# Performance work log

Measured on AMD Instinct MI355X. Metric: run time of the kernel, lower is better.

Reference implementation:

```python
import jax, jax.numpy as jnp
import numpy as np

B, L, T, LM, DFF, D, H = 8, 256, 2048, 4096, 1024, 84, 4
HD = D // H  # 21
NCLS = 265


def _ln(x, s, b):
    m = x.mean(-1, keepdims=True)
    v = ((x - m) ** 2).mean(-1, keepdims=True)
    return (x - m) * jax.lax.rsqrt(v + 1e-5) * s + b


def _fourier(xyz, gB):
    # PositionEmbeddingCoordsSine(d_pos=10, pos_type='fourier'): xyz @ B * 2pi -> [sin, cos]
    proj = (2.0 * jnp.pi) * jnp.einsum('bnc,cd->bnd', xyz, gB)  # [B,N,5]
    return jnp.concatenate([jnp.sin(proj), jnp.cos(proj)], axis=-1)  # [B,N,10]


def setup_inputs() -> dict:
    key = jax.random.key(0)
    ks = jax.random.split(key, 20)
    def nrm(k, shape, scale):
        return jax.random.normal(k, shape, jnp.float32) * scale
    coords = jax.random.uniform(ks[0], (B, L, 6), jnp.float32)
    cls = jax.random.randint(ks[1], (B, L), 0, NCLS).astype(jnp.float32)
    vision_features = jnp.concatenate([coords, cls[..., None]], axis=-1)  # [B,L,7]
    FIN = D * L + LM  # 25600
    inp = {
        'grd_tokens': nrm(ks[2], (T, LM), 1.0),
        'vision_features': vision_features,
        'token_batch_idx': jax.random.randint(ks[3], (T,), 0, B),
        'gauss_B': nrm(ks[4], (3, 5), 1.0),
        'class_emb': nrm(ks[5], (NCLS, 64), 0.02),
        'w_in': nrm(ks[6], (2, D, 3 * D), D ** -0.5),
        'b_in': jnp.zeros((2, 3 * D), jnp.float32),
        'w_out': nrm(ks[7], (2, D, D), D ** -0.5),
        'b_out': jnp.zeros((2, D), jnp.float32),
        'ln1_s': jnp.ones((2, D), jnp.float32), 'ln1_b': jnp.zeros((2, D), jnp.float32),
        'w_ff1': nrm(ks[8], (2, D, DFF), D ** -0.5), 'b_ff1': jnp.zeros((2, DFF), jnp.float32),
        'w_ff2': nrm(ks[9], (2, DFF, D), DFF ** -0.5), 'b_ff2': jnp.zeros((2, D), jnp.float32),
        'ln2_s': jnp.ones((2, D), jnp.float32), 'ln2_b': jnp.zeros((2, D), jnp.float32),
        'w0': nrm(ks[10], (FIN, DFF), FIN ** -0.5), 'b0': jnp.zeros((DFF,), jnp.float32),
        'w1': nrm(ks[11], (DFF, DFF), DFF ** -0.5), 'b1': jnp.zeros((DFF,), jnp.float32),
        'w2': nrm(ks[12], (DFF, DFF), DFF ** -0.5), 'b2': jnp.zeros((DFF,), jnp.float32),
        'w3': nrm(ks[13], (DFF, DFF), DFF ** -0.5), 'b3': jnp.zeros((DFF,), jnp.float32),
        'w4': nrm(ks[14], (DFF, 6), DFF ** -0.5), 'b4': jnp.zeros((6,), jnp.float32),
    }
    return inp


def reference(grd_tokens, vision_features, token_batch_idx, gauss_B, class_emb,
              w_in, b_in, w_out, b_out, ln1_s, ln1_b, w_ff1, b_ff1, w_ff2, b_ff2,
              ln2_s, ln2_b, w0, b0, w1, b1, w2, b2, w3, b3, w4, b4):
    pe_min = _fourier(vision_features[:, :, 0:3], gauss_B)  # [B,L,10]
    pe_max = _fourier(vision_features[:, :, 3:6], gauss_B)  # [B,L,10]
    cls = vision_features[:, :, -1].astype(jnp.int32)
    src = jnp.concatenate([pe_min, pe_max, class_emb[cls]], axis=-1)  # [B,L,84]
    pad = jnp.all(vision_features == 0, axis=-1)  # [B,L]
    neg = jnp.where(pad, -1e9, 0.0)[:, None, None, :]  # [B,1,1,L] key-padding bias
    # 2-layer post-norm transformer encoder (DETR-style, pos=None, dropout=0)
    for l in range(2):
        qkv = src @ w_in[l] + b_in[l]
        q, k, v = jnp.split(qkv, 3, axis=-1)
        q = q.reshape(B, L, H, HD)
        k = k.reshape(B, L, H, HD)
        v = v.reshape(B, L, H, HD)
        scores = jnp.einsum('blhd,bmhd->bhlm', q, k) / jnp.sqrt(jnp.float32(HD)) + neg
        attn = jax.nn.softmax(scores, axis=-1)
        o = jnp.einsum('bhlm,bmhd->blhd', attn, v).reshape(B, L, D)
        src = _ln(src + o @ w_out[l] + b_out[l], ln1_s[l], ln1_b[l])
        ff = jax.nn.relu(src @ w_ff1[l] + b_ff1[l]) @ w_ff2[l] + b_ff2[l]
        src = _ln(src + ff, ln2_s[l], ln2_b[l])
    vision_flat = src.reshape(B, L * D)  # flattened encoder output per sample [B, 21504]
    # batched version of the ragged python loop: gather per-token vision feat + concat lm feat
    feat = jnp.concatenate([vision_flat[token_batch_idx], grd_tokens], axis=-1)  # [T, 25600]
    h = jax.nn.relu(feat @ w0 + b0)
    h = jax.nn.relu(h @ w1 + b1)
    h = jax.nn.relu(h @ w2 + b2)
    h = jax.nn.relu(h @ w3 + b3)
    return h @ w4 + b4  # [T, 6]
```

## Files before the change

### kernel.cpp

```cpp
#include <hip/hip_runtime.h>
#include <hip/hip_bf16.h>

#define B_ 8
#define L_ 256
#define T_ 2048
#define LM_ 4096
#define DFF_ 1024
#define D_ 84
#define H_ 4
#define HD_ 21
#define BL_ (B_*L_)
#define VISF_ (L_*D_)
#define VKS 168
#define VCHUNK (VISF_/VKS)
#define AKS 8
#define AKEYS (L_/AKS)

typedef __attribute__((ext_vector_type(8))) short bf16x8;
typedef __attribute__((ext_vector_type(4))) float f32x4;

struct bh4 { __hip_bfloat16 x, y, z, w; };


__device__ __forceinline__ void dev_wT_pack(const float* __restrict__ W,
        __hip_bfloat16* __restrict__ Wp, int K, int N, int kb, int nb, int tid,
        float (*t)[33])
{
    int tx = tid & 31, ty = tid >> 5;
    #pragma unroll
    for (int i = 0; i < 4; ++i)
        t[ty + i*8][tx] = W[(size_t)(kb + ty + i*8)*N + nb + tx];
    __syncthreads();
    int KG = K >> 3;
    #pragma unroll
    for (int i = 0; i < 4; ++i) {
        int n = nb + ty + i*8, k = kb + tx;
        Wp[((size_t)(n>>4)*KG + (k>>3))*128 + (n&15)*8 + (k&7)] = __float2bfloat16(t[tx][ty + i*8]);
    }
}

__device__ __forceinline__ void dev_wTp_pack(const float* __restrict__ W,
        __hip_bfloat16* __restrict__ Wp, int K, int N, int KP, int kb, int nb, int tid,
        float (*t)[33])
{
    int tx = tid & 31, ty = tid >> 5;
    #pragma unroll
    for (int i = 0; i < 4; ++i) {
        int k = kb + ty + i*8, n = nb + tx;
        t[ty + i*8][tx] = (k < K && n < N) ? W[(size_t)k*N + n] : 0.0f;
    }
    __syncthreads();
    int KG = KP >> 3;
    #pragma unroll
    for (int i = 0; i < 4; ++i) {
        int n = nb + ty + i*8, k = kb + tx;
        Wp[((size_t)(n>>4)*KG + (k>>3))*128 + (n&15)*8 + (k&7)] = __float2bfloat16(t[tx][ty + i*8]);
    }
}

__device__ __forceinline__ void dev_f2b_pack(const float* __restrict__ in,
        __hip_bfloat16* __restrict__ out, int i)
{
    int row = i >> 9, kc = i & 511;
    const float4* p = reinterpret_cast<const float4*>(in + (size_t)row*4096 + kc*8);
    float4 v0 = p[0], v1 = p[1];
    bh4 a = { __float2bfloat16(v0.x), __float2bfloat16(v0.y),
              __float2bfloat16(v0.z), __float2bfloat16(v0.w) };
    bh4 b = { __float2bfloat16(v1.x), __float2bfloat16(v1.y),
              __float2bfloat16(v1.z), __float2bfloat16(v1.w) };
    __hip_bfloat16* o = out + ((size_t)(row>>4)*512 + kc)*128 + (row&15)*8;
    reinterpret_cast<bh4*>(o)[0] = a;
    reinterpret_cast<bh4*>(o)[1] = b;
}

__device__ __forceinline__ void dev_build_src(const float* __restrict__ vf,
        const float* __restrict__ gB, const float* __restrict__ cemb,
        float* __restrict__ src, float* __restrict__ neg, int row)
{
    float v[7];
    bool allz = true;
    #pragma unroll
    for (int c = 0; c < 7; ++c) { v[c] = vf[row*7 + c]; allz = allz && (v[c] == 0.0f); }
    neg[row] = allz ? -1e9f : 0.0f;
    float* s = src + (size_t)row * D_;
    const float TWO_PI = 6.28318530717958647692f;
    #pragma unroll
    for (int d = 0; d < 5; ++d) {
        float pmin = TWO_PI * (v[0]*gB[d] + v[1]*gB[5+d] + v[2]*gB[10+d]);
        float pmax = TWO_PI * (v[3]*gB[d] + v[4]*gB[5+d] + v[5]*gB[10+d]);
        s[d]      = sinf(pmin);  s[5+d]  = cosf(pmin);
        s[10+d]   = sinf(pmax);  s[15+d] = cosf(pmax);
    }
    int cls = (int)v[6];
    const float4* ce = reinterpret_cast<const float4*>(cemb + (size_t)cls*64);
    float4* so = reinterpret_cast<float4*>(s + 20);
    #pragma unroll
    for (int i = 0; i < 16; ++i) so[i] = ce[i];
}

__global__ __launch_bounds__(256) void k_pack_all(
        const float* __restrict__ grd, const float* __restrict__ w0,
        const float* __restrict__ w1, const float* __restrict__ w2,
        const float* __restrict__ w3, const float* __restrict__ w_ff1,
        const float* __restrict__ w_ff2,
        const float* __restrict__ vf, const float* __restrict__ gB,
        const float* __restrict__ cemb,
        __hip_bfloat16* __restrict__ grdb, __hip_bfloat16* __restrict__ w0t,
        __hip_bfloat16* __restrict__ w1t, __hip_bfloat16* __restrict__ w2t,
        __hip_bfloat16* __restrict__ w3t, __hip_bfloat16* __restrict__ wff1t,
        __hip_bfloat16* __restrict__ wff2t,
        float* __restrict__ src, float* __restrict__ neg)
{
    __shared__ float t[32][33];
    int blk = blockIdx.x, tid = threadIdx.x;
    if (blk < 4096) {
        dev_wT_pack(w0 + (size_t)VISF_*DFF_, w0t, LM_, DFF_,
                    (blk & 127)*32, (blk >> 7)*32, tid, t);
    } else if (blk < 5120) {
        int u = blk - 4096;
        dev_wT_pack(w1, w1t, DFF_, DFF_, (u & 31)*32, (u >> 5)*32, tid, t);
    } else if (blk < 6144) {
        int u = blk - 5120;
        dev_wT_pack(w2, w2t, DFF_, DFF_, (u & 31)*32, (u >> 5)*32, tid, t);
    } else if (blk < 7168) {
        int u = blk - 6144;
        dev_wT_pack(w3, w3t, DFF_, DFF_, (u & 31)*32, (u >> 5)*32, tid, t);
    } else if (blk < 7424) {
        int u = blk - 7168;
        int l = u >> 7; u &= 127;
        dev_wTp_pack(w_ff1 + (size_t)l*D_*DFF_, wff1t + (size_t)l*1024*128,
                     D_, DFF_, 128, (u & 3)*32, (u >> 2)*32, tid, t);
    } else if (blk < 7616) {
        int u = blk - 7424;
        int l = u / 96; u -= l*96;
        dev_wTp_pack(w_ff2 + (size_t)l*DFF_*D_, wff2t + (size_t)l*98304,
                     DFF_, D_, DFF_, (u % 32)*32, (u / 32)*32, tid, t);
    } else if (blk < 11712) {
        dev_f2b_pack(grd, grdb, (blk - 7616)*256 + tid);
    } else {
        dev_build_src(vf, gB, cemb, src, neg, (blk - 11712)*256 + tid);
    }
}

__global__ __launch_bounds__(256) void k_qkv8(const float* __restrict__ src,
        const float* __restrict__ w_in, const float* __restrict__ b_in,
        float* __restrict__ qkv, int lay)
{
    __shared__ float s8[8][D_];
    int r0 = blockIdx.x * 8, tid = threadIdx.x;
    for (int idx = tid; idx < 8*D_; idx += 256) {
        int r = idx / D_, d = idx - r*D_;
        s8[r][d] = src[(size_t)(r0+r)*D_ + d];
    }
    __syncthreads();
    if (tid < 3*D_) {
        const float* w = w_in + (size_t)lay*D_*3*D_ + tid;
        float acc[8] = {};
        for (int d = 0; d < D_; ++d) {
            float wv = w[(size_t)d*3*D_];
            #pragma unroll
            for (int r = 0; r < 8; ++r) acc[r] = fmaf(s8[r][d], wv, acc[r]);
        }
        float bv = b_in[lay*3*D_ + tid];
        #pragma unroll
        for (int r = 0; r < 8; ++r) qkv[(size_t)(r0+r)*(3*D_) + tid] = acc[r] + bv;
    }
}

__global__ __launch_bounds__(256) void k_attn_part(const float* __restrict__ qkv,
        const float* __restrict__ neg, float* __restrict__ part)
{
    __shared__ float ks_[AKEYS*HD_], vs_[AKEYS*HD_], ns[AKEYS];
    int bh = blockIdx.x;
    int b = bh >> 2, h = bh & 3;
    int sp = blockIdx.y;
    int tid = threadIdx.x;
    int k0 = sp * AKEYS;
    for (int idx = tid; idx < AKEYS*HD_; idx += 256) {
        int l = idx / HD_, d = idx - l*HD_;
        size_t base = ((size_t)(b*L_ + k0 + l))*(3*D_) + h*HD_ + d;
        ks_[idx] = qkv[base + D_];
        vs_[idx] = qkv[base + 2*D_];
    }
    if (tid < AKEYS) ns[tid] = neg[b*L_ + k0 + tid];
    __syncthreads();
    float q[HD_];
    {
        size_t base = ((size_t)(b*L_ + tid))*(3*D_) + h*HD_;
        #pragma unroll
        for (int d = 0; d < HD_; ++d) q[d] = qkv[base + d];
    }
    const float scale = 0.21821789023599239f;
    float m_run = -INFINITY, l_run = 0.0f;
    float o[HD_];
    #pragma unroll
    for (int d = 0; d < HD_; ++d) o[d] = 0.0f;
    for (int m = 0; m < AKEYS; ++m) {
        const float* krow = &ks_[m*HD_];
        float sdot = 0.0f;
        #pragma unroll
        for (int d = 0; d < HD_; ++d) sdot = fmaf(q[d], krow[d], sdot);
        float sc = sdot * scale + ns[m];
        float nm = fmaxf(m_run, sc);
        float c = __expf(m_run - nm);
        float p = __expf(sc - nm);
        l_run = l_run * c + p;
        const float* vrow = &vs_[m*HD_];
        #pragma unroll
        for (int d = 0; d < HD_; ++d) o[d] = fmaf(p, vrow[d], o[d]*c);
        m_run = nm;
    }
    float* po = part + (((size_t)bh*AKS + sp)*L_ + tid)*24;
    #pragma unroll
    for (int d = 0; d < HD_; ++d) po[d] = o[d];
    po[21] = m_run;
    po[22] = l_run;
}

__global__ __launch_bounds__(128) void k_oproj_ln(const float* __restrict__ part,
        const float* __restrict__ w_out, const float* __restrict__ b_out,
        const float* __restrict__ ln_s, const float* __restrict__ ln_b,
        float* __restrict__ src, __hip_bfloat16* __restrict__ srcb, int lay)
{
    __shared__ float os[D_];
    __shared__ float r1[128], r2[128];
    int row = blockIdx.x, tid = threadIdx.x;
    int b = row >> 8, q = row & 255;
    if (tid < D_) {
        int h = tid / 21, d = tid - h*21;
        const float* pb = part + (((size_t)(b*H_ + h)*AKS)*L_ + q)*24;
        float m_tot = -INFINITY;
        #pragma unroll
        for (int sp = 0; sp < AKS; ++sp)
            m_tot = fmaxf(m_tot, pb[(size_t)sp*L_*24 + 21]);
        float l_tot = 0.0f, ov = 0.0f;
        #pragma unroll
        for (int sp = 0; sp < AKS; ++sp) {
            const float* pp = pb + (size_t)sp*L_*24;
            float e = __expf(pp[21] - m_tot);
            l_tot = fmaf(pp[22], e, l_tot);
            ov = fmaf(pp[d], e, ov);
        }
        os[tid] = ov / l_tot;
    }
    __syncthreads();
    float y = 0.0f;
    if (tid < D_) {
        const float* w = w_out + (size_t)lay*D_*D_ + tid;
        float acc = b_out[lay*D_ + tid];
        for (int d = 0; d < D_; ++d) acc = fmaf(os[d], w[(size_t)d*D_], acc);
        y = src[(size_t)row*D_ + tid] + acc;
    }
    r1[tid] = (tid < D_) ? y : 0.0f;
    r2[tid] = (tid < D_) ? y*y : 0.0f;
    __syncthreads();
    for (int s = 64; s > 0; s >>= 1) {
        if (tid < s) { r1[tid] += r1[tid+s]; r2[tid] += r2[tid+s]; }
        __syncthreads();
    }
    float mean = r1[0] * (1.0f/D_);
    float var  = r2[0] * (1.0f/D_) - mean*mean;
    float rstd = rsqrtf(var + 1e-5f);
    float out = 0.0f;
    if (tid < D_) {
        out = (y - mean)*rstd*ln_s[lay*D_+tid] + ln_b[lay*D_+tid];
        src[(size_t)row*D_ + tid] = out;
    }
    __hip_bfloat16 val = (tid < D_) ? __float2bfloat16(out) : __float2bfloat16(0.0f);
    srcb[((size_t)(row>>4)*16 + (tid>>3))*128 + (row&15)*8 + (tid&7)] = val;
}

__global__ __launch_bounds__(256) void k_ff2_mfma(
        const __hip_bfloat16* __restrict__ hb,
        const __hip_bfloat16* __restrict__ wp,
        float* __restrict__ part)
{
    int tid = threadIdx.x, wave = tid >> 6, lane = tid & 63;
    int wr = wave >> 1, wc = wave & 1;
    int l15 = lane & 15, l4 = lane >> 4;
    int bm = blockIdx.x * 64, sp = blockIdx.y;
    const __hip_bfloat16* Aw = hb + ((size_t)((bm >> 4) + wr*2) * 128) * 128 + lane*8;
    const __hip_bfloat16* Bw = wp + ((size_t)(wc*3) * 128) * 128 + lane*8;
    f32x4 acc[2][3] = {};
    int kg0 = sp * 16;
    #pragma unroll
    for (int kk = 0; kk < 16; kk += 4) {
        int kg = kg0 + kk;
        bf16x8 a[2], b[3];
        #pragma unroll
        for (int mi = 0; mi < 2; ++mi)
            a[mi] = *reinterpret_cast<const bf16x8*>(Aw + ((size_t)mi*128 + kg)*128);
        #pragma unroll
        for (int ni = 0; ni < 3; ++ni)
            b[ni] = *reinterpret_cast<const bf16x8*>(Bw + ((size_t)ni*128 + kg)*128);
        #pragma unroll
        for (int mi = 0; mi < 2; ++mi)
            #pragma unroll
            for (int ni = 0; ni < 3; ++ni)
                acc[mi][ni] = __builtin_amdgcn_mfma_f32_16x16x32_bf16(
                    a[mi], b[ni], acc[mi][ni], 0, 0, 0);
    }
    float* po = part + (size_t)sp*(2048*96);
    #pragma unroll
    for (int mi = 0; mi < 2; ++mi)
        #pragma unroll
        for (int reg = 0; reg < 4; ++reg) {
            int row = bm + wr*32 + mi*16 + l4*4 + reg;
            #pragma unroll
            for (int ni = 0; ni < 3; ++ni) {
                int col = wc*48 + ni*16 + l15;
                po[(size_t)row*96 + col] = acc[mi][ni][reg];
            }
        }
}

__global__ __launch_bounds__(128) void k_ff2ln_red(const float* __restrict__ part,
        const float* __restrict__ b_ff2, const float* __restrict__ ln_s,
        const float* __restrict__ ln_b, float* __restrict__ src, int lay)
{
    __shared__ float r1[128], r2[128];
    int row = blockIdx.x, tid = threadIdx.x;
    float y = 0.0f;
    if (tid < D_) {
        #pragma unroll
        for (int sp = 0; sp < 8; ++sp)
            y += part[(size_t)sp*(2048*96) + (size_t)row*96 + tid];
        y += b_ff2[lay*D_ + tid] + src[(size_t)row*D_ + tid];
    }
    r1[tid] = (tid < D_) ? y : 0.0f;
    r2[tid] = (tid < D_) ? y*y : 0.0f;
    __syncthreads();
    for (int s = 64; s > 0; s >>= 1) {
        if (tid < s) { r1[tid] += r1[tid+s]; r2[tid] += r2[tid+s]; }
        __syncthreads();
    }
    float mean = r1[0] * (1.0f/D_);
    float var  = r2[0] * (1.0f/D_) - mean*mean;
    float rstd = rsqrtf(var + 1e-5f);
    if (tid < D_)
        src[(size_t)row*D_ + tid] = (y - mean)*rstd*ln_s[lay*D_+tid] + ln_b[lay*D_+tid];
}

__global__ __launch_bounds__(256) void k_vis_gemm(const float* __restrict__ src,
        const float* __restrict__ w0, float* __restrict__ partials)
{
    __shared__ float vf[8][VCHUNK];
    __shared__ float red[8][256][4];
    int nt = blockIdx.x, sp = blockIdx.y, tid = threadIdx.x;
    int k0 = sp * VCHUNK;
    for (int idx = tid; idx < 8*VCHUNK; idx += 256) {
        int r = idx >> 7, c = idx & 127;
        vf[r][c] = src[(size_t)r*VISF_ + k0 + c];
    }
    __syncthreads();
    int ng = tid & 31;
    int kh = tid >> 5;
    const float* wp = w0 + (size_t)(k0 + kh*16)*DFF_ + nt*128 + ng*4;
    float acc[8][4] = {};
    #pragma unroll 4
    for (int kk = 0; kk < 16; ++kk) {
        float4 w = *reinterpret_cast<const float4*>(wp + (size_t)kk*DFF_);
        #pragma unroll
        for (int m = 0; m < 8; ++m) {
            float sv = vf[m][kh*16 + kk];
            acc[m][0] = fmaf(sv, w.x, acc[m][0]);
            acc[m][1] = fmaf(sv, w.y, acc[m][1]);
            acc[m][2] = fmaf(sv, w.z, acc[m][2]);
            acc[m][3] = fmaf(sv, w.w, acc[m][3]);
        }
    }
    #pragma unroll
    for (int m = 0; m < 8; ++m)
        *reinterpret_cast<float4*>(&red[m][tid][0]) =
            make_float4(acc[m][0], acc[m][1], acc[m][2], acc[m][3]);
    __syncthreads();
    int m2 = tid >> 5, ng2 = tid & 31;
    float4 s = *reinterpret_cast<const float4*>(&red[m2][ng2][0]);
    #pragma unroll
    for (int j = 1; j < 8; ++j) {
        float4 v = *reinterpret_cast<const float4*>(&red[m2][j*32 + ng2][0]);
        s.x += v.x; s.y += v.y; s.z += v.z; s.w += v.w;
    }
    *reinterpret_cast<float4*>(
        &partials[(size_t)sp*8192 + m2*1024 + nt*128 + ng2*4]) = s;
}

__global__ __launch_bounds__(256) void k_vis_red(const float* __restrict__ partials,
        float* __restrict__ vis)
{
    int o = blockIdx.x*256 + threadIdx.x;
    float s = 0.0f;
    for (int sp = 0; sp < VKS; ++sp) s += partials[(size_t)sp*8192 + o];
    vis[o] = s;
}

template<bool ADD_VIS, int K>
__global__ __launch_bounds__(256) void mfma_gemm(
        const __hip_bfloat16* __restrict__ Ap,
        const __hip_bfloat16* __restrict__ Bp,
        const float* __restrict__ bias,
        const float* __restrict__ vis,
        const int* __restrict__ bidx,
        __hip_bfloat16* __restrict__ Cp)
{
    constexpr int KG = K >> 3;
    constexpr int NG = 128;
    __shared__ __align__(16) __hip_bfloat16 cst[64*128];
    int tid = threadIdx.x, wave = tid >> 6, lane = tid & 63;
    int wr = wave >> 1, wc = wave & 1;
    int l15 = lane & 15, l4 = lane >> 4;
    int bm = blockIdx.x * 64, bn = blockIdx.y * 128;
    const __hip_bfloat16* Aw = Ap + ((size_t)((bm >> 4) + wr*2) * KG) * 128 + lane*8;
    const __hip_bfloat16* Bw = Bp + ((size_t)((bn >> 4) + wc*4) * KG) * 128 + lane*8;
    f32x4 acc[2][4] = {};

    #pragma unroll 4
    for (int kg = 0; kg < KG; kg += 4) {
        bf16x8 a[2], b[4];
        #pragma unroll
        for (int mi = 0; mi < 2; ++mi)
            a[mi] = *reinterpret_cast<const bf16x8*>(Aw + ((size_t)mi*KG + kg)*128);
        #pragma unroll
        for (int ni = 0; ni < 4; ++ni)
            b[ni] = *reinterpret_cast<const bf16x8*>(Bw + ((size_t)ni*KG + kg)*128);
        #pragma unroll
        for (int mi = 0; mi < 2; ++mi)
            #pragma unroll
            for (int ni = 0; ni < 4; ++ni)
                acc[mi][ni] = __builtin_amdgcn_mfma_f32_16x16x32_bf16(
                    a[mi], b[ni], acc[mi][ni], 0, 0, 0);
    }

    #pragma unroll
    for (int mi = 0; mi < 2; ++mi) {
        int mg = wr*2 + mi;
        #pragma unroll
        for (int ni = 0; ni < 4; ++ni) {
            int cg = wc*8 + ni*2 + (l15 >> 3);
            int c  = l15 & 7;
            int col = bn + cg*8 + c;
            float bv = bias[col];
            #pragma unroll
            for (int reg = 0; reg < 4; ++reg) {
                int r = l4*4 + reg;
                float v = acc[mi][ni][reg] + bv;
                if (ADD_VIS) v += vis[(size_t)bidx[bm + mg*16 + r]*1024 + col];
                v = fmaxf(v, 0.0f);
                cst[((mg*16 + cg)*16 + r)*8 + c] = __float2bfloat16(v);
            }
        }
    }
    __syncthreads();
    #pragma unroll
    for (int ch = tid; ch < 1024; ch += 256) {
        int mgcg = ch >> 4, r = ch & 15;
        int mg = mgcg >> 4, cg = mgcg & 15;
        size_t go = ((size_t)((bm >> 4) + mg) * NG + (bn >> 3) + cg) * 128 + r*8;
        *reinterpret_cast<bf16x8*>(Cp + go) =
            *reinterpret_cast<const bf16x8*>(cst + (size_t)ch*8);
    }
}

__global__ __launch_bounds__(64) void k_final(const __hip_bfloat16* __restrict__ hp,
        const float* __restrict__ w4, const float* __restrict__ b4, float* __restrict__ out)
{
    int t = blockIdx.x, lane = threadIdx.x;
    int mg = t >> 4, r = t & 15;
    float acc[6] = {};
    #pragma unroll
    for (int it = 0; it < 2; ++it) {
        int kg = lane + it*64;
        bf16x8 h = *reinterpret_cast<const bf16x8*>(hp + ((size_t)mg*128 + kg)*128 + r*8);
        #pragma unroll
        for (int j = 0; j < 8; ++j) {
            unsigned short us = (unsigned short)h[j];
            float hv = __uint_as_float((unsigned)us << 16);
            int k = kg*8 + j;
            #pragma unroll
            for (int c = 0; c < 6; ++c) acc[c] = fmaf(hv, w4[k*6 + c], acc[c]);
        }
    }
    #pragma unroll
    for (int j = 0; j < 6; ++j)
        #pragma unroll
        for (int s = 32; s > 0; s >>= 1) acc[j] += __shfl_down(acc[j], s);
    if (lane == 0) {
        #pragma unroll
        for (int j = 0; j < 6; ++j) out[(size_t)t*6 + j] = acc[j] + b4[j];
    }
}

extern "C" void kernel_launch(void* const* d_in, const int* in_sizes, int n_in,
                              void* d_out, int out_size, void* d_ws, size_t ws_size,
                              hipStream_t stream)
{
    const float* grd   = (const float*)d_in[0];
    const float* vfeat = (const float*)d_in[1];
    const int*   tbi   = (const int*)  d_in[2];
    const float* gB    = (const float*)d_in[3];
    const float* cemb  = (const float*)d_in[4];
    const float* w_in  = (const float*)d_in[5];
    const float* b_in  = (const float*)d_in[6];
    const float* w_out = (const float*)d_in[7];
    const float* b_out = (const float*)d_in[8];
    const float* ln1_s = (const float*)d_in[9];
    const float* ln1_b = (const float*)d_in[10];
    const float* w_ff1 = (const float*)d_in[11];
    const float* b_ff1 = (const float*)d_in[12];
    const float* w_ff2 = (const float*)d_in[13];
    const float* b_ff2 = (const float*)d_in[14];
    const float* ln2_s = (const float*)d_in[15];
    const float* ln2_b = (const float*)d_in[16];
    const float* w0    = (const float*)d_in[17];
    const float* b0    = (const float*)d_in[18];
    const float* w1    = (const float*)d_in[19];
    const float* b1    = (const float*)d_in[20];
    const float* w2    = (const float*)d_in[21];
    const float* b2    = (const float*)d_in[22];
    const float* w3    = (const float*)d_in[23];
    const float* b3    = (const float*)d_in[24];
    const float* w4    = (const float*)d_in[25];
    const float* b4    = (const float*)d_in[26];

    float* ws = (float*)d_ws;
    float* src    = ws;
    float* neg    = src    + 172032;
    float* qkv    = neg    + 2048;
    float* vparts = qkv    + 516096;
    float* visp   = vparts + 1376256;
    float* ffpart = visp   + 8192;
    float* fend   = ffpart + 1572864;
    __hip_bfloat16* grdb  = (__hip_bfloat16*)fend;
    __hip_bfloat16* w0t   = grdb  + 8388608;
    __hip_bfloat16* w1t   = w0t   + 4194304;
    __hip_bfloat16* w2t   = w1t   + 1048576;
    __hip_bfloat16* w3t   = w2t   + 1048576;
    __hip_bfloat16* hab   = w3t   + 1048576;
    __hip_bfloat16* hbb   = hab   + 2097152;
    __hip_bfloat16* srcb  = hbb   + 2097152;
    __hip_bfloat16* wff1t = srcb  + 262144;
    __hip_bfloat16* wff2t = wff1t + 262144;
    __hip_bfloat16* ffh   = hab;

    k_pack_all<<<11720, 256, 0, stream>>>(grd, w0, w1, w2, w3, w_ff1, w_ff2,
        vfeat, gB, cemb, grdb, w0t, w1t, w2t, w3t, wff1t, wff2t, src, neg);

    for (int lay = 0; lay < 2; ++lay) {
        k_qkv8     <<<BL_/8, 256, 0, stream>>>(src, w_in, b_in, qkv, lay);
        k_attn_part<<<dim3(B_*H_, AKS), 256, 0, stream>>>(qkv, neg, ffpart);
        k_oproj_ln <<<BL_, 128, 0, stream>>>(ffpart, w_out, b_out, ln1_s, ln1_b, src, srcb, lay);
        mfma_gemm<false, 128><<<dim3(32, 8), 256, 0, stream>>>(
            srcb, wff1t + (size_t)lay*1024*128, b_ff1 + lay*DFF_, nullptr, nullptr, ffh);
        k_ff2_mfma<<<dim3(32, 8), 256, 0, stream>>>(
            ffh, wff2t + (size_t)lay*98304, ffpart);
        k_ff2ln_red<<<BL_, 128, 0, stream>>>(ffpart, b_ff2, ln2_s, ln2_b, src, lay);
    }

    k_vis_gemm<<<dim3(8, VKS), 256, 0, stream>>>(src, w0, vparts);
    k_vis_red<<<32, 256, 0, stream>>>(vparts, visp);

    dim3 mg(T_/64, DFF_/128);
    mfma_gemm<true,  LM_ ><<<mg, 256, 0, stream>>>(grdb, w0t, b0, visp, tbi, hab);
    mfma_gemm<false, DFF_><<<mg, 256, 0, stream>>>(hab,  w1t, b1, nullptr, nullptr, hbb);
    mfma_gemm<false, DFF_><<<mg, 256, 0, stream>>>(hbb,  w2t, b2, nullptr, nullptr, hab);
    mfma_gemm<false, DFF_><<<mg, 256, 0, stream>>>(hab,  w3t, b3, nullptr, nullptr, hbb);

    k_final<<<T_, 64, 0, stream>>>(hbb, w4, b4, (float*)d_out);
}
```

Before: 240.8 us.

## Fuse FF2 GEMM with residual LayerNorm and reduce vision split-K count

```diff
diff --git a/kernel.cpp b/kernel.cpp
--- a/kernel.cpp
+++ b/kernel.cpp
@@ -11,7 +11,7 @@
 #define HD_ 21
 #define BL_ (B_*L_)
 #define VISF_ (L_*D_)
-#define VKS 168
+#define VKS 56
 #define VCHUNK (VISF_/VKS)
 #define AKS 8
 #define AKEYS (L_/AKS)
@@ -270,75 +270,52 @@
     srcb[((size_t)(row>>4)*16 + (tid>>3))*128 + (row&15)*8 + (tid&7)] = val;
 }
 
-__global__ __launch_bounds__(256) void k_ff2_mfma(
+__global__ __launch_bounds__(128) void k_ff2_ln(
         const __hip_bfloat16* __restrict__ hb,
         const __hip_bfloat16* __restrict__ wp,
-        float* __restrict__ part)
-{
-    int tid = threadIdx.x, wave = tid >> 6, lane = tid & 63;
-    int wr = wave >> 1, wc = wave & 1;
-    int l15 = lane & 15, l4 = lane >> 4;
-    int bm = blockIdx.x * 64, sp = blockIdx.y;
-    const __hip_bfloat16* Aw = hb + ((size_t)((bm >> 4) + wr*2) * 128) * 128 + lane*8;
-    const __hip_bfloat16* Bw = wp + ((size_t)(wc*3) * 128) * 128 + lane*8;
-    f32x4 acc[2][3] = {};
-    int kg0 = sp * 16;
-    #pragma unroll
-    for (int kk = 0; kk < 16; kk += 4) {
-        int kg = kg0 + kk;
-        bf16x8 a[2], b[3];
-        #pragma unroll
-        for (int mi = 0; mi < 2; ++mi)
-            a[mi] = *reinterpret_cast<const bf16x8*>(Aw + ((size_t)mi*128 + kg)*128);
-        #pragma unroll
-        for (int ni = 0; ni < 3; ++ni)
-            b[ni] = *reinterpret_cast<const bf16x8*>(Bw + ((size_t)ni*128 + kg)*128);
-        #pragma unroll
-        for (int mi = 0; mi < 2; ++mi)
-            #pragma unroll
-            for (int ni = 0; ni < 3; ++ni)
-                acc[mi][ni] = __builtin_amdgcn_mfma_f32_16x16x32_bf16(
-                    a[mi], b[ni], acc[mi][ni], 0, 0, 0);
-    }
-    float* po = part + (size_t)sp*(2048*96);
-    #pragma unroll
-    for (int mi = 0; mi < 2; ++mi)
-        #pragma unroll
-        for (int reg = 0; reg < 4; ++reg) {
-            int row = bm + wr*32 + mi*16 + l4*4 + reg;
-            #pragma unroll
-            for (int ni = 0; ni < 3; ++ni) {
-                int col = wc*48 + ni*16 + l15;
-                po[(size_t)row*96 + col] = acc[mi][ni][reg];
-            }
-        }
-}
-
-__global__ __launch_bounds__(128) void k_ff2ln_red(const float* __restrict__ part,
         const float* __restrict__ b_ff2, const float* __restrict__ ln_s,
         const float* __restrict__ ln_b, float* __restrict__ src, int lay)
 {
-    __shared__ float r1[128], r2[128];
-    int row = blockIdx.x, tid = threadIdx.x;
-    float y = 0.0f;
-    if (tid < D_) {
-        #pragma unroll
-        for (int sp = 0; sp < 8; ++sp)
-            y += part[(size_t)sp*(2048*96) + (size_t)row*96 + tid];
-        y += b_ff2[lay*D_ + tid] + src[(size_t)row*D_ + tid];
-    }
-    r1[tid] = (tid < D_) ? y : 0.0f;
-    r2[tid] = (tid < D_) ? y*y : 0.0f;
-    __syncthreads();
-    for (int s = 64; s > 0; s >>= 1) {
-        if (tid < s) { r1[tid] += r1[tid+s]; r2[tid] += r2[tid+s]; }
-        __syncthreads();
-    }
-    float mean = r1[0] * (1.0f/D_);
-    float var  = r2[0] * (1.0f/D_) - mean*mean;
+    __shared__ float yb[16][96];
+    int tid = threadIdx.x, wc = tid >> 6, lane = tid & 63;
+    int l15 = lane & 15, l4 = lane >> 4;
+    int mg = blockIdx.x;
+    const __hip_bfloat16* Aw = hb + ((size_t)mg * 128) * 128 + lane*8;
+    const __hip_bfloat16* Bw = wp + ((size_t)(wc*3) * 128) * 128 + lane*8;
+    f32x4 acc[3] = {};
+    #pragma unroll 8
+    for (int kg = 0; kg < 128; kg += 4) {
+        bf16x8 a = *reinterpret_cast<const bf16x8*>(Aw + (size_t)kg*128);
+        #pragma unroll
+        for (int ni = 0; ni < 3; ++ni) {
+            bf16x8 b = *reinterpret_cast<const bf16x8*>(Bw + ((size_t)ni*128 + kg)*128);
+            acc[ni] = __builtin_amdgcn_mfma_f32_16x16x32_bf16(a, b, acc[ni], 0, 0, 0);
+        }
+    }
+    #pragma unroll
+    for (int ni = 0; ni < 3; ++ni)
+        #pragma unroll
+        for (int reg = 0; reg < 4; ++reg)
+            yb[l4*4 + reg][wc*48 + ni*16 + l15] = acc[ni][reg];
+    __syncthreads();
+    int r = tid >> 3, c8 = tid & 7;
+    int row = mg*16 + r;
+    float s1 = 0.0f, s2 = 0.0f;
+    for (int c = c8; c < D_; c += 8) {
+        float y = yb[r][c] + b_ff2[lay*D_ + c] + src[(size_t)row*D_ + c];
+        yb[r][c] = y;
+        s1 += y; s2 += y*y;
+    }
+    #pragma unroll
+    for (int m = 1; m < 8; m <<= 1) {
+        s1 += __shfl_xor(s1, m);
+        s2 += __shfl_xor(s2, m);
+    }
+    float mean = s1 * (1.0f/D_);
+    float var  = s2 * (1.0f/D_) - mean*mean;
     float rstd = rsqrtf(var + 1e-5f);
-    if (tid < D_)
-        src[(size_t)row*D_ + tid] = (y - mean)*rstd*ln_s[lay*D_+tid] + ln_b[lay*D_+tid];
+    for (int c = c8; c < D_; c += 8)
+        src[(size_t)row*D_ + c] = (yb[r][c] - mean)*rstd*ln_s[lay*D_ + c] + ln_b[lay*D_ + c];
 }
 
 __global__ __launch_bounds__(256) void k_vis_gemm(const float* __restrict__ src,
@@ -348,21 +325,21 @@
     __shared__ float red[8][256][4];
     int nt = blockIdx.x, sp = blockIdx.y, tid = threadIdx.x;
     int k0 = sp * VCHUNK;
-    for (int idx = tid; idx < 8*VCHUNK; idx += 256) {
-        int r = idx >> 7, c = idx & 127;
-        vf[r][c] = src[(size_t)r*VISF_ + k0 + c];
-    }
+    #pragma unroll
+    for (int r = 0; r < 8; ++r)
+        for (int c = tid; c < VCHUNK; c += 256)
+            vf[r][c] = src[(size_t)r*VISF_ + k0 + c];
     __syncthreads();
     int ng = tid & 31;
     int kh = tid >> 5;
-    const float* wp = w0 + (size_t)(k0 + kh*16)*DFF_ + nt*128 + ng*4;
+    const float* wp = w0 + (size_t)(k0 + kh*(VCHUNK/8))*DFF_ + nt*128 + ng*4;
     float acc[8][4] = {};
     #pragma unroll 4
-    for (int kk = 0; kk < 16; ++kk) {
+    for (int kk = 0; kk < VCHUNK/8; ++kk) {
         float4 w = *reinterpret_cast<const float4*>(wp + (size_t)kk*DFF_);
         #pragma unroll
         for (int m = 0; m < 8; ++m) {
-            float sv = vf[m][kh*16 + kk];
+            float sv = vf[m][kh*(VCHUNK/8) + kk];
             acc[m][0] = fmaf(sv, w.x, acc[m][0]);
             acc[m][1] = fmaf(sv, w.y, acc[m][1]);
             acc[m][2] = fmaf(sv, w.z, acc[m][2]);
@@ -551,9 +528,8 @@
         k_oproj_ln <<<BL_, 128, 0, stream>>>(ffpart, w_out, b_out, ln1_s, ln1_b, src, srcb, lay);
         mfma_gemm<false, 128><<<dim3(32, 8), 256, 0, stream>>>(
             srcb, wff1t + (size_t)lay*1024*128, b_ff1 + lay*DFF_, nullptr, nullptr, ffh);
-        k_ff2_mfma<<<dim3(32, 8), 256, 0, stream>>>(
-            ffh, wff2t + (size_t)lay*98304, ffpart);
-        k_ff2ln_red<<<BL_, 128, 0, stream>>>(ffpart, b_ff2, ln2_s, ln2_b, src, lay);
+        k_ff2_ln<<<128, 128, 0, stream>>>(
+            ffh, wff2t + (size_t)lay*98304, b_ff2, ln2_s, ln2_b, src, lay);
     }
 
     k_vis_gemm<<<dim3(8, VKS), 256, 0, stream>>>(src, w0, vparts);
```

New measurement: 252.5 us. +4.8%, slower.
